# Optimization experiments

Hardware: AMD Instinct MI355X
Metric: run time of the kernel (lower is better)

Reference implementation:

```python
import jax, jax.numpy as jnp
import numpy as np

B, T, DMODEL = 8, 1024, 1024
N_HEADS, DK, DV = 16, 64, 64
FF_INNER = 4096


def setup_inputs() -> dict:
    key = jax.random.key(0)
    ks = jax.random.split(key, 9)
    s = 0.02  # init scale so softmax logits stay sane
    return {
        "x": jax.random.normal(ks[0], (B, T, DMODEL), dtype=jnp.float32),
        "Wq": jax.random.normal(ks[1], (N_HEADS, DMODEL, DK), dtype=jnp.float32) * s,
        "Wk": jax.random.normal(ks[2], (N_HEADS, DMODEL, DK), dtype=jnp.float32) * s,
        "Wv": jax.random.normal(ks[3], (N_HEADS, DMODEL, DV), dtype=jnp.float32) * s,
        "Wo": jax.random.normal(ks[4], (DMODEL, DMODEL), dtype=jnp.float32) * s,
        "W1": jax.random.normal(ks[5], (FF_INNER, DMODEL), dtype=jnp.float32) * s,
        "b1": jax.random.normal(ks[6], (FF_INNER,), dtype=jnp.float32) * s,
        "W2": jax.random.normal(ks[7], (DMODEL, FF_INNER), dtype=jnp.float32) * s,
        "b2": jax.random.normal(ks[8], (DMODEL,), dtype=jnp.float32) * s,
    }


def _pseudo_norm(y):
    # Original: y - mean - std (unbiased std, torch default). NOT a real layernorm.
    mean = jnp.mean(y, axis=-1, keepdims=True)
    std = jnp.std(y, axis=-1, keepdims=True, ddof=1)
    return y - mean - std


def reference(x, Wq, Wk, Wv, Wo, W1, b1, W2, b2):
    dk = Wq.shape[-1]
    # per-head projections: (B,T,D) x (H,D,dk) -> (B,H,T,dk)
    WQ = jnp.einsum("btd,hdk->bhtk", x, Wq)
    WK = jnp.einsum("btd,hdk->bhtk", x, Wk)
    WV = jnp.einsum("btd,hdv->bhtv", x, Wv)
    scores = jnp.einsum("bhqk,bhsk->bhqs", WQ, WK) / np.sqrt(dk).astype(np.float32)
    # Faithful to original: softmax over dim=2, i.e. the QUERY axis of (B,H,Tq,Tk)
    attn = jax.nn.softmax(scores, axis=2)
    part = jnp.einsum("bhqs,bhsv->bhqv", attn, WV)  # (B,H,T,dv)
    # concat heads: (B,T,H*dv) == (B,T,dmodel)
    part = part.transpose(0, 2, 1, 3).reshape(part.shape[0], part.shape[2], -1)
    out1 = part @ Wo + x
    out1 = _pseudo_norm(out1)
    # FeedForward: Linear(dmodel->inner), relu, Linear(inner->dmodel)
    h = jnp.maximum(out1 @ W1.T + b1, 0.0)
    out2 = h @ W2.T + b2 + out1
    return _pseudo_norm(out2)
```

## Files before the change

### kernel.cpp

```cpp
#include <hip/hip_runtime.h>
#include <math.h>


#define B_ 8
#define T_ 1024
#define D_ 1024
#define H_ 16
#define DK_ 64
#define FF_ 4096
#define M_ (B_ * T_)

typedef unsigned short u16;
typedef __attribute__((ext_vector_type(8))) short bf16x8;
typedef __attribute__((ext_vector_type(4))) float f32x4;

#define QSZ 8388608ull

__device__ __forceinline__ float b2f(u16 u) {
  union { unsigned int i; float f; } x;
  x.i = ((unsigned int)u) << 16;
  return x.f;
}
__device__ __forceinline__ u16 f2b(float f) {
  union { float f; unsigned int i; } x;
  x.f = f;
  unsigned int r = (x.i + 0x7FFFu + ((x.i >> 16) & 1u)) >> 16;
  return (u16)r;
}
__device__ __forceinline__ float fexp2(float x) {
#if __has_builtin(__builtin_amdgcn_exp2f)
  return __builtin_amdgcn_exp2f(x);
#else
  return exp2f(x);
#endif
}
#define C_QK 0.1803368801111244f

typedef __attribute__((address_space(1))) const void gas_void;
typedef __attribute__((address_space(3))) void las_void;
__device__ __forceinline__ void gload16(const void* g, void* l) {
  __builtin_amdgcn_global_load_lds((gas_void*)g, (las_void*)l, 16, 0, 0);
}

template <int EPI>
__global__ __launch_bounds__(256) void gemm16_k(
    const u16* __restrict__ A, const u16* __restrict__ Bt,
    int M, int N, int K, int lda, int ldb,
    float* __restrict__ C, int ldc, u16* __restrict__ Cb,
    const float* __restrict__ res, const float* __restrict__ bias) {
  __shared__ __align__(16) u16 As[2][128 * 32];
  __shared__ __align__(16) u16 Bs[2][128 * 32];

  const int tid = threadIdx.x;
  const int lane = tid & 63, wv = tid >> 6;
  const int m0 = blockIdx.y * 128, n0 = blockIdx.x * 128;
  const int wr = (wv >> 1) * 64, wc = (wv & 1) * 64;

  f32x4 acc[4][4];
#pragma unroll
  for (int i = 0; i < 4; ++i)
#pragma unroll
    for (int j = 0; j < 4; ++j) acc[i][j] = (f32x4){0.f, 0.f, 0.f, 0.f};

  const int srow = wv * 16 + (lane >> 2);
  const int scol = (lane & 3) * 8;
  const int fr = lane & 15, fk = (lane >> 4) * 8;

  const u16* gA0 = &A[(size_t)(m0 + srow) * lda + scol];
  const u16* gA1 = &A[(size_t)(m0 + srow + 64) * lda + scol];
  const u16* gB0 = &Bt[(size_t)(n0 + srow) * ldb + scol];
  const u16* gB1 = &Bt[(size_t)(n0 + srow + 64) * ldb + scol];

  gload16(gA0, &As[0][wv * 512]);
  gload16(gA1, &As[0][2048 + wv * 512]);
  gload16(gB0, &Bs[0][wv * 512]);
  gload16(gB1, &Bs[0][2048 + wv * 512]);
  __syncthreads();

  int cur = 0;
  for (int k0 = 0; k0 < K; k0 += 32) {
    if (k0 + 32 < K) {
      int nx = cur ^ 1, ko = k0 + 32;
      gload16(gA0 + ko, &As[nx][wv * 512]);
      gload16(gA1 + ko, &As[nx][2048 + wv * 512]);
      gload16(gB0 + ko, &Bs[nx][wv * 512]);
      gload16(gB1 + ko, &Bs[nx][2048 + wv * 512]);
    }
    bf16x8 af[4], bfr[4];
#pragma unroll
    for (int mi = 0; mi < 4; ++mi)
      af[mi] = *(const bf16x8*)&As[cur][(wr + mi * 16 + fr) * 32 + fk];
#pragma unroll
    for (int ni = 0; ni < 4; ++ni)
      bfr[ni] = *(const bf16x8*)&Bs[cur][(wc + ni * 16 + fr) * 32 + fk];
#pragma unroll
    for (int mi = 0; mi < 4; ++mi)
#pragma unroll
      for (int ni = 0; ni < 4; ++ni)
        acc[mi][ni] = __builtin_amdgcn_mfma_f32_16x16x32_bf16(
            af[mi], bfr[ni], acc[mi][ni], 0, 0, 0);
    __syncthreads();
    cur ^= 1;
  }

  const int fq = (lane >> 4) * 4;
#pragma unroll
  for (int mi = 0; mi < 4; ++mi) {
#pragma unroll
    for (int ni = 0; ni < 4; ++ni) {
      const int row = m0 + wr + mi * 16 + fq;
      const int col = n0 + wc + ni * 16 + fr;
      f32x4 v = acc[mi][ni];
      if (EPI == 6) {
        const int seg = col >> 10, cl = col & 1023;
        if (seg < 2) {
          u16* dst = Cb + (size_t)seg * QSZ;
#pragma unroll
          for (int r = 0; r < 4; ++r)
            dst[(size_t)(row + r) * 1024 + cl] = f2b(v[r]);
        } else {
          ushort4 w;
          w.x = f2b(v[0]); w.y = f2b(v[1]); w.z = f2b(v[2]); w.w = f2b(v[3]);
          size_t vidx = 2 * QSZ +
                        (((size_t)(row >> 10) * 16 + (cl >> 6)) * 64 +
                         (cl & 63)) * (size_t)T_ + (row & 1023);
          *(ushort4*)&Cb[vidx] = w;
        }
      } else {
#pragma unroll
        for (int r = 0; r < 4; ++r) {
          float val = v[r];
          size_t idx = (size_t)(row + r) * ldc + col;
          if (EPI == 1) {
            C[idx] = val + res[idx];
          } else if (EPI == 2) {
            Cb[idx] = f2b(fmaxf(val + bias[col], 0.f));
          } else if (EPI == 3) {
            C[idx] = val + bias[col] + res[idx];
          } else if (EPI == 4) {
            C[idx] = C[idx] + val;
          }
        }
      }
    }
  }
}

__global__ __launch_bounds__(256) void cvt_k(const float* __restrict__ in,
                                             u16* __restrict__ out, int n4) {
  int i = blockIdx.x * 256 + threadIdx.x;
  if (i >= n4) return;
  float4 v = *(const float4*)&in[(size_t)i * 4];
  ushort4 o;
  o.x = f2b(v.x); o.y = f2b(v.y); o.z = f2b(v.z); o.w = f2b(v.w);
  *(ushort4*)&out[(size_t)i * 4] = o;
}

__global__ __launch_bounds__(256) void tconv_k(const float* __restrict__ src,
                                               u16* __restrict__ dst, int R,
                                               int C) {
  __shared__ __align__(16) float t[32][33];
  const size_t bo = (size_t)blockIdx.z * R * C;
  const int r0 = blockIdx.y * 32, c0 = blockIdx.x * 32;
  const int tid = threadIdx.x;
  const int row = tid >> 3, c4 = (tid & 7) * 4;
  float4 v = *(const float4*)&src[bo + (size_t)(r0 + row) * C + c0 + c4];
  t[row][c4 + 0] = v.x; t[row][c4 + 1] = v.y;
  t[row][c4 + 2] = v.z; t[row][c4 + 3] = v.w;
  __syncthreads();
  ushort4 o;
  o.x = f2b(t[c4 + 0][row]); o.y = f2b(t[c4 + 1][row]);
  o.z = f2b(t[c4 + 2][row]); o.w = f2b(t[c4 + 3][row]);
  *(ushort4*)&dst[bo + (size_t)(c0 + row) * R + r0 + c4] = o;
}

__global__ __launch_bounds__(256) void attn_lsum_k(
    const u16* __restrict__ q, const u16* __restrict__ k,
    float* __restrict__ Lg) {
  __shared__ __align__(16) u16 Qs[128 * 64];
  __shared__ float Lsh[2][128];
  const int tid = threadIdx.x, lane = tid & 63, wv = tid >> 6;
  const int s0 = blockIdx.x * 128, h = blockIdx.y, b = blockIdx.z;
  const int bh = b * H_ + h;
  const u16* qbase = q + (size_t)b * T_ * D_ + h * DK_;
  const u16* kbase = k + (size_t)b * T_ * D_ + h * DK_;

  const int wr = (wv >> 1) * 64, wc = (wv & 1) * 64;
  const int fr = lane & 15, fs8 = (lane >> 4) * 8, fq = (lane >> 4) * 4;

  bf16x8 kf[4][2];
#pragma unroll
  for (int mi = 0; mi < 4; ++mi)
#pragma unroll
    for (int ks = 0; ks < 2; ++ks)
      kf[mi][ks] = *(const bf16x8*)&kbase[(size_t)(s0 + wr + mi * 16 + fr) * D_ +
                                          ks * 32 + fs8];

  float lrun[4][4];
#pragma unroll
  for (int mi = 0; mi < 4; ++mi)
#pragma unroll
    for (int r = 0; r < 4; ++r) lrun[mi][r] = 0.f;

  const int srow = wv * 8 + (lane >> 3);
  const int sscol = ((lane & 7) ^ ((lane >> 3) & 7)) * 8;

  for (int q0 = 0; q0 < T_; q0 += 128) {
    __syncthreads();
#pragma unroll
    for (int it = 0; it < 4; ++it)
      gload16(&qbase[(size_t)(q0 + it * 32 + srow) * D_ + sscol],
              &Qs[(it * 32 + wv * 8) * 64]);
    __syncthreads();

    f32x4 acc[4][4];
#pragma unroll
    for (int mi = 0; mi < 4; ++mi)
#pragma unroll
      for (int ni = 0; ni < 4; ++ni) acc[mi][ni] = (f32x4){0.f, 0.f, 0.f, 0.f};

#pragma unroll
    for (int ks = 0; ks < 2; ++ks) {
      bf16x8 qf[4];
#pragma unroll
      for (int ni = 0; ni < 4; ++ni) {
        int qr = wc + ni * 16 + fr;
        int slot = (ks * 4 + (lane >> 4)) ^ (qr & 7);
        qf[ni] = *(const bf16x8*)&Qs[qr * 64 + slot * 8];
      }
#pragma unroll
      for (int mi = 0; mi < 4; ++mi)
#pragma unroll
        for (int ni = 0; ni < 4; ++ni)
          acc[mi][ni] = __builtin_amdgcn_mfma_f32_16x16x32_bf16(
              kf[mi][ks], qf[ni], acc[mi][ni], 0, 0, 0);
    }
#pragma unroll
    for (int mi = 0; mi < 4; ++mi)
#pragma unroll
      for (int r = 0; r < 4; ++r) {
        float e = 0.f;
#pragma unroll
        for (int ni = 0; ni < 4; ++ni) e += fexp2(acc[mi][ni][r] * C_QK);
        lrun[mi][r] += e;
      }
  }

#pragma unroll
  for (int mi = 0; mi < 4; ++mi)
#pragma unroll
    for (int r = 0; r < 4; ++r) {
      float s = lrun[mi][r];
      s += __shfl_xor(s, 1, 64); s += __shfl_xor(s, 2, 64);
      s += __shfl_xor(s, 4, 64); s += __shfl_xor(s, 8, 64);
      if (fr == 0) Lsh[wv & 1][wr + mi * 16 + fq + r] = s;
    }
  __syncthreads();
  if (tid < 128)
    Lg[(size_t)bh * T_ + s0 + tid] = -__log2f(Lsh[0][tid] + Lsh[1][tid]);
}

__global__ __launch_bounds__(256) void attn_pv_k(
    const u16* __restrict__ q, const u16* __restrict__ k,
    const u16* __restrict__ vt, const float* __restrict__ Lg,
    u16* __restrict__ part) {
  __shared__ __align__(16) u16 Ks[128 * 64];
  __shared__ __align__(16) u16 Vs[64 * 128];
  __shared__ __align__(16) u16 Ps[128 * 128];
  const int tid = threadIdx.x, lane = tid & 63, wv = tid >> 6;
  const int q0 = blockIdx.x * 128, h = blockIdx.y, b = blockIdx.z;
  const int bh = b * H_ + h;
  const u16* qbase = q + (size_t)b * T_ * D_ + h * DK_;
  const u16* kbase = k + (size_t)b * T_ * D_ + h * DK_;
  const u16* vtb = vt + (size_t)bh * DK_ * T_;
  const float* lb = Lg + (size_t)bh * T_;

  const int wr = (wv >> 1) * 64, wc = (wv & 1) * 64;
  const int fr = lane & 15, fs8 = (lane >> 4) * 8, fq = (lane >> 4) * 4;

  bf16x8 qf[4][2];
#pragma unroll
  for (int mi = 0; mi < 4; ++mi)
#pragma unroll
    for (int ks = 0; ks < 2; ++ks)
      qf[mi][ks] = *(const bf16x8*)&qbase[(size_t)(q0 + wr + mi * 16 + fr) * D_ +
                                          ks * 32 + fs8];

  f32x4 acc2[2][4];
#pragma unroll
  for (int i = 0; i < 2; ++i)
#pragma unroll
    for (int j = 0; j < 4; ++j) acc2[i][j] = (f32x4){0.f, 0.f, 0.f, 0.f};

  const int ksrow = wv * 8 + (lane >> 3);
  const int kscol = ((lane & 7) ^ ((lane >> 3) & 7)) * 8;

  for (int s0 = 0; s0 < T_; s0 += 128) {
    __syncthreads();
#pragma unroll
    for (int it = 0; it < 4; ++it)
      gload16(&kbase[(size_t)(s0 + it * 32 + ksrow) * D_ + kscol],
              &Ks[(it * 32 + wv * 8) * 64]);
#pragma unroll
    for (int it = 0; it < 4; ++it) {
      int v = it * 16 + wv * 4 + (lane >> 4);
      int sslot = (lane & 15) ^ (v & 7);
      gload16(&vtb[(size_t)v * T_ + s0 + sslot * 8],
              &Vs[(it * 16 + wv * 4) * 128]);
    }
    __syncthreads();

    f32x4 accs[4][4];
#pragma unroll
    for (int mi = 0; mi < 4; ++mi)
#pragma unroll
      for (int ni = 0; ni < 4; ++ni) accs[mi][ni] = (f32x4){0.f, 0.f, 0.f, 0.f};
#pragma unroll
    for (int ks = 0; ks < 2; ++ks) {
      bf16x8 kfr[4];
#pragma unroll
      for (int ni = 0; ni < 4; ++ni) {
        int sr = wc + ni * 16 + fr;
        int slot = (ks * 4 + (lane >> 4)) ^ (sr & 7);
        kfr[ni] = *(const bf16x8*)&Ks[sr * 64 + slot * 8];
      }
#pragma unroll
      for (int mi = 0; mi < 4; ++mi)
#pragma unroll
        for (int ni = 0; ni < 4; ++ni)
          accs[mi][ni] = __builtin_amdgcn_mfma_f32_16x16x32_bf16(
              qf[mi][ks], kfr[ni], accs[mi][ni], 0, 0, 0);
    }

#pragma unroll
    for (int ni = 0; ni < 4; ++ni) {
      float lg = lb[s0 + wc + ni * 16 + fr];
      int scol = wc + ni * 16 + fr;
#pragma unroll
      for (int mi = 0; mi < 4; ++mi) {
#pragma unroll
        for (int r = 0; r < 4; ++r) {
          int qrow = wr + mi * 16 + fq + r;
          u16 pv = f2b(fexp2(fmaf(accs[mi][ni][r], C_QK, lg)));
          int eoff = qrow * 128 + ((((scol << 1) ^ ((qrow & 7) << 4))) >> 1);
          Ps[eoff] = pv;
        }
      }
    }
    __syncthreads();

#pragma unroll
    for (int ks2 = 0; ks2 < 4; ++ks2) {
      bf16x8 pa[2], vb2[4];
#pragma unroll
      for (int mi2 = 0; mi2 < 2; ++mi2) {
        int qr = wv * 32 + mi2 * 16 + fr;
        int slot = (ks2 * 4 + (lane >> 4)) ^ (qr & 7);
        pa[mi2] = *(const bf16x8*)&Ps[qr * 128 + slot * 8];
      }
#pragma unroll
      for (int ni2 = 0; ni2 < 4; ++ni2) {
        int v = ni2 * 16 + fr;
        int slot = (ks2 * 4 + (lane >> 4)) ^ (v & 7);
        vb2[ni2] = *(const bf16x8*)&Vs[v * 128 + slot * 8];
      }
#pragma unroll
      for (int mi2 = 0; mi2 < 2; ++mi2)
#pragma unroll
        for (int ni2 = 0; ni2 < 4; ++ni2)
          acc2[mi2][ni2] = __builtin_amdgcn_mfma_f32_16x16x32_bf16(
              pa[mi2], vb2[ni2], acc2[mi2][ni2], 0, 0, 0);
    }
  }

#pragma unroll
  for (int mi2 = 0; mi2 < 2; ++mi2)
#pragma unroll
    for (int ni2 = 0; ni2 < 4; ++ni2)
#pragma unroll
      for (int r = 0; r < 4; ++r) {
        int qrow = q0 + wv * 32 + mi2 * 16 + fq + r;
        int v = ni2 * 16 + fr;
        part[(size_t)(b * T_ + qrow) * D_ + h * DK_ + v] =
            f2b(acc2[mi2][ni2][r]);
      }
}

template <bool WB>
__global__ __launch_bounds__(256) void norm_k(const float* __restrict__ in,
                                              float* __restrict__ out,
                                              u16* __restrict__ ob) {
  __shared__ float red[8];
  const int row = blockIdx.x, tid = threadIdx.x;
  float4 vv = *(const float4*)&in[(size_t)row * D_ + tid * 4];
  float s = vv.x + vv.y + vv.z + vv.w;
  for (int off = 1; off < 64; off <<= 1) s += __shfl_xor(s, off, 64);
  if ((tid & 63) == 0) red[tid >> 6] = s;
  __syncthreads();
  float mean = (red[0] + red[1] + red[2] + red[3]) * (1.f / 1024.f);
  float dx = vv.x - mean, dy = vv.y - mean, dz = vv.z - mean, dw = vv.w - mean;
  float s2 = dx * dx + dy * dy + dz * dz + dw * dw;
  __syncthreads();
  for (int off = 1; off < 64; off <<= 1) s2 += __shfl_xor(s2, off, 64);
  if ((tid & 63) == 0) red[4 + (tid >> 6)] = s2;
  __syncthreads();
  float var = (red[4] + red[5] + red[6] + red[7]) * (1.f / 1023.f);
  float sd = sqrtf(var);
  float4 o = {dx - sd, dy - sd, dz - sd, dw - sd};
  *(float4*)&out[(size_t)row * D_ + tid * 4] = o;
  if (WB) {
    ushort4 q;
    q.x = f2b(o.x); q.y = f2b(o.y); q.z = f2b(o.z); q.w = f2b(o.w);
    *(ushort4*)&ob[(size_t)row * D_ + tid * 4] = q;
  }
}

extern "C" void kernel_launch(void* const* d_in, const int* in_sizes, int n_in,
                              void* d_out, int out_size, void* d_ws,
                              size_t ws_size, hipStream_t stream) {
  const float* x  = (const float*)d_in[0];
  const float* Wq = (const float*)d_in[1];
  const float* Wk = (const float*)d_in[2];
  const float* Wv = (const float*)d_in[3];
  const float* Wo = (const float*)d_in[4];
  const float* W1 = (const float*)d_in[5];
  const float* b1 = (const float*)d_in[6];
  const float* W2 = (const float*)d_in[7];
  const float* b2 = (const float*)d_in[8];

  char* w = (char*)d_ws;
  u16* qb16   = (u16*)(w + (0ull << 20));
  u16* kb16   = (u16*)(w + (16ull << 20));
  u16* Vt     = (u16*)(w + (32ull << 20));
  u16* xb     = (u16*)(w + (48ull << 20));
  u16* part16 = (u16*)(w + (64ull << 20));
  u16* Wqkv   = (u16*)(w + (80ull << 20));
  u16* Wot    = (u16*)(w + (86ull << 20));
  u16* W1b    = (u16*)(w + (88ull << 20));
  u16* W2b    = (u16*)(w + (96ull << 20));
  float* Lg   = (float*)(w + (104ull << 20));
  u16* o1b = qb16;
  u16* hc  = kb16;
  float* o1 = (float*)d_out;

  dim3 thr(256);

  int n4x = (M_ * D_) / 4;
  cvt_k<<<dim3((n4x + 255) / 256), thr, 0, stream>>>(x, xb, n4x);
  tconv_k<<<dim3(2, 32, 16), thr, 0, stream>>>(Wq, Wqkv, 1024, 64);
  tconv_k<<<dim3(2, 32, 16), thr, 0, stream>>>(Wk, Wqkv + 1048576, 1024, 64);
  tconv_k<<<dim3(2, 32, 16), thr, 0, stream>>>(Wv, Wqkv + 2097152, 1024, 64);
  tconv_k<<<dim3(32, 32, 1), thr, 0, stream>>>(Wo, Wot, 1024, 1024);
  int n4w = (FF_ * D_) / 4;
  cvt_k<<<dim3((n4w + 255) / 256), thr, 0, stream>>>(W1, W1b, n4w);
  cvt_k<<<dim3((n4w + 255) / 256), thr, 0, stream>>>(W2, W2b, n4w);

  gemm16_k<6><<<dim3(3072 / 128, M_ / 128), thr, 0, stream>>>(
      xb, Wqkv, M_, 3072, D_, D_, D_, nullptr, D_, qb16, nullptr, nullptr);

  dim3 ga(T_ / 128, H_, B_);
  attn_lsum_k<<<ga, thr, 0, stream>>>(qb16, kb16, Lg);
  attn_pv_k<<<ga, thr, 0, stream>>>(qb16, kb16, Vt, Lg, part16);

  gemm16_k<1><<<dim3(D_ / 128, M_ / 128), thr, 0, stream>>>(
      part16, Wot, M_, D_, D_, D_, D_, o1, D_, nullptr, x, nullptr);
  norm_k<true><<<dim3(M_), thr, 0, stream>>>(o1, o1, o1b);

  for (int c = 0; c < 2; ++c) {
    const u16* W1c = W1b + (size_t)c * 2048 * 1024;
    const u16* W2c = W2b + (size_t)c * 2048;
    gemm16_k<2><<<dim3(2048 / 128, M_ / 128), thr, 0, stream>>>(
        o1b, W1c, M_, 2048, 1024, 1024, 1024, nullptr, 2048, hc, nullptr,
        b1 + c * 2048);
    if (c == 0) {
      gemm16_k<3><<<dim3(D_ / 128, M_ / 128), thr, 0, stream>>>(
          hc, W2c, M_, 1024, 2048, 2048, FF_, o1, D_, nullptr, o1, b2);
    } else {
      gemm16_k<4><<<dim3(D_ / 128, M_ / 128), thr, 0, stream>>>(
          hc, W2c, M_, 1024, 2048, 2048, FF_, o1, D_, nullptr, nullptr, nullptr);
    }
  }

  norm_k<false><<<dim3(M_), thr, 0, stream>>>(o1, o1, nullptr);
}
```

Measured before the change: 649.2 us.

## Fold softmax column normalizer into V and transpose score MFMA for packed P stores

Instead of adding -log2(L) inside every exponent in the PV kernel, the lsum kernel now stores the reciprocal column sums and a new pass pre-scales V^T by them in place. The score MFMA operands are swapped so each lane holds four consecutive key positions, letting P be written to LDS as packed 8-byte stores with a new XOR swizzle instead of scalar 2-byte stores. It also swaps the manual bf16 rounding for the HIP intrinsic. The extra elementwise pass over V and the extra bf16 rounding of scaled V add traffic and slight numerical change.

```diff
diff --git a/kernel.cpp b/kernel.cpp
--- a/kernel.cpp
+++ b/kernel.cpp
@@ -1,4 +1,5 @@
 #include <hip/hip_runtime.h>
+#include <hip/hip_bf16.h>
 #include <math.h>
 
 
@@ -22,10 +23,8 @@
   return x.f;
 }
 __device__ __forceinline__ u16 f2b(float f) {
-  union { float f; unsigned int i; } x;
-  x.f = f;
-  unsigned int r = (x.i + 0x7FFFu + ((x.i >> 16) & 1u)) >> 16;
-  return (u16)r;
+  __hip_bfloat16 h = __float2bfloat16(f);
+  return *(u16*)&h;
 }
 __device__ __forceinline__ float fexp2(float x) {
 #if __has_builtin(__builtin_amdgcn_exp2f)
@@ -176,7 +175,7 @@
 
 __global__ __launch_bounds__(256) void attn_lsum_k(
     const u16* __restrict__ q, const u16* __restrict__ k,
-    float* __restrict__ Lg) {
+    float* __restrict__ Lrcp) {
   __shared__ __align__(16) u16 Qs[128 * 64];
   __shared__ float Lsh[2][128];
   const int tid = threadIdx.x, lane = tid & 63, wv = tid >> 6;
@@ -257,13 +256,31 @@
     }
   __syncthreads();
   if (tid < 128)
-    Lg[(size_t)bh * T_ + s0 + tid] = -__log2f(Lsh[0][tid] + Lsh[1][tid]);
+    Lrcp[(size_t)bh * T_ + s0 + tid] = 1.f / (Lsh[0][tid] + Lsh[1][tid]);
+}
+
+__global__ __launch_bounds__(256) void vscale_k(u16* __restrict__ vt,
+                                                const float* __restrict__ Lrcp) {
+  int i8 = blockIdx.x * 256 + threadIdx.x;
+  size_t base = (size_t)i8 * 8;
+  int bh = (int)(base >> 16);
+  int s = (int)(base & 1023);
+  float4 r0 = *(const float4*)&Lrcp[(size_t)bh * 1024 + s];
+  float4 r1 = *(const float4*)&Lrcp[(size_t)bh * 1024 + s + 4];
+  ushort4 a = *(const ushort4*)&vt[base];
+  ushort4 c = *(const ushort4*)&vt[base + 4];
+  ushort4 oa, oc;
+  oa.x = f2b(b2f(a.x) * r0.x); oa.y = f2b(b2f(a.y) * r0.y);
+  oa.z = f2b(b2f(a.z) * r0.z); oa.w = f2b(b2f(a.w) * r0.w);
+  oc.x = f2b(b2f(c.x) * r1.x); oc.y = f2b(b2f(c.y) * r1.y);
+  oc.z = f2b(b2f(c.z) * r1.z); oc.w = f2b(b2f(c.w) * r1.w);
+  *(ushort4*)&vt[base] = oa;
+  *(ushort4*)&vt[base + 4] = oc;
 }
 
 __global__ __launch_bounds__(256) void attn_pv_k(
     const u16* __restrict__ q, const u16* __restrict__ k,
-    const u16* __restrict__ vt, const float* __restrict__ Lg,
-    u16* __restrict__ part) {
+    const u16* __restrict__ vt, u16* __restrict__ part) {
   __shared__ __align__(16) u16 Ks[128 * 64];
   __shared__ __align__(16) u16 Vs[64 * 128];
   __shared__ __align__(16) u16 Ps[128 * 128];
@@ -273,17 +290,16 @@
   const u16* qbase = q + (size_t)b * T_ * D_ + h * DK_;
   const u16* kbase = k + (size_t)b * T_ * D_ + h * DK_;
   const u16* vtb = vt + (size_t)bh * DK_ * T_;
-  const float* lb = Lg + (size_t)bh * T_;
 
   const int wr = (wv >> 1) * 64, wc = (wv & 1) * 64;
   const int fr = lane & 15, fs8 = (lane >> 4) * 8, fq = (lane >> 4) * 4;
 
   bf16x8 qf[4][2];
 #pragma unroll
-  for (int mi = 0; mi < 4; ++mi)
+  for (int ni = 0; ni < 4; ++ni)
 #pragma unroll
     for (int ks = 0; ks < 2; ++ks)
-      qf[mi][ks] = *(const bf16x8*)&qbase[(size_t)(q0 + wr + mi * 16 + fr) * D_ +
+      qf[ni][ks] = *(const bf16x8*)&qbase[(size_t)(q0 + wc + ni * 16 + fr) * D_ +
                                           ks * 32 + fs8];
 
   f32x4 acc2[2][4];
@@ -310,41 +326,43 @@
     }
     __syncthreads();
 
-    f32x4 accs[4][4];
+    f32x4 st[4][4];
 #pragma unroll
     for (int mi = 0; mi < 4; ++mi)
 #pragma unroll
-      for (int ni = 0; ni < 4; ++ni) accs[mi][ni] = (f32x4){0.f, 0.f, 0.f, 0.f};
+      for (int ni = 0; ni < 4; ++ni) st[mi][ni] = (f32x4){0.f, 0.f, 0.f, 0.f};
 #pragma unroll
     for (int ks = 0; ks < 2; ++ks) {
-      bf16x8 kfr[4];
-#pragma unroll
-      for (int ni = 0; ni < 4; ++ni) {
-        int sr = wc + ni * 16 + fr;
+      bf16x8 kfa[4];
+#pragma unroll
+      for (int mi = 0; mi < 4; ++mi) {
+        int sr = wr + mi * 16 + fr;
         int slot = (ks * 4 + (lane >> 4)) ^ (sr & 7);
-        kfr[ni] = *(const bf16x8*)&Ks[sr * 64 + slot * 8];
+        kfa[mi] = *(const bf16x8*)&Ks[sr * 64 + slot * 8];
       }
 #pragma unroll
       for (int mi = 0; mi < 4; ++mi)
 #pragma unroll
         for (int ni = 0; ni < 4; ++ni)
-          accs[mi][ni] = __builtin_amdgcn_mfma_f32_16x16x32_bf16(
-              qf[mi][ks], kfr[ni], accs[mi][ni], 0, 0, 0);
+          st[mi][ni] = __builtin_amdgcn_mfma_f32_16x16x32_bf16(
+              kfa[mi], qf[ni][ks], st[mi][ni], 0, 0, 0);
     }
 
 #pragma unroll
     for (int ni = 0; ni < 4; ++ni) {
-      float lg = lb[s0 + wc + ni * 16 + fr];
-      int scol = wc + ni * 16 + fr;
+      int qcol = wc + ni * 16 + fr;
 #pragma unroll
       for (int mi = 0; mi < 4; ++mi) {
-#pragma unroll
-        for (int r = 0; r < 4; ++r) {
-          int qrow = wr + mi * 16 + fq + r;
-          u16 pv = f2b(fexp2(fmaf(accs[mi][ni][r], C_QK, lg)));
-          int eoff = qrow * 128 + ((((scol << 1) ^ ((qrow & 7) << 4))) >> 1);
-          Ps[eoff] = pv;
-        }
+        int sb = wr + mi * 16 + fq;
+        u16 e0 = f2b(fexp2(st[mi][ni][0] * C_QK));
+        u16 e1 = f2b(fexp2(st[mi][ni][1] * C_QK));
+        u16 e2 = f2b(fexp2(st[mi][ni][2] * C_QK));
+        u16 e3 = f2b(fexp2(st[mi][ni][3] * C_QK));
+        uint2 w;
+        w.x = (unsigned int)e0 | ((unsigned int)e1 << 16);
+        w.y = (unsigned int)e2 | ((unsigned int)e3 << 16);
+        int byte = qcol * 256 + ((sb * 2) ^ ((qcol & 15) << 4));
+        *(uint2*)((char*)Ps + byte) = w;
       }
     }
     __syncthreads();
@@ -355,8 +373,8 @@
 #pragma unroll
       for (int mi2 = 0; mi2 < 2; ++mi2) {
         int qr = wv * 32 + mi2 * 16 + fr;
-        int slot = (ks2 * 4 + (lane >> 4)) ^ (qr & 7);
-        pa[mi2] = *(const bf16x8*)&Ps[qr * 128 + slot * 8];
+        int byte = qr * 256 + (((ks2 * 32 + (lane >> 4) * 8) * 2) ^ ((qr & 15) << 4));
+        pa[mi2] = *(const bf16x8*)((const char*)Ps + byte);
       }
 #pragma unroll
       for (int ni2 = 0; ni2 < 4; ++ni2) {
@@ -438,7 +456,7 @@
   u16* Wot    = (u16*)(w + (86ull << 20));
   u16* W1b    = (u16*)(w + (88ull << 20));
   u16* W2b    = (u16*)(w + (96ull << 20));
-  float* Lg   = (float*)(w + (104ull << 20));
+  float* Lrcp = (float*)(w + (104ull << 20));
   u16* o1b = qb16;
   u16* hc  = kb16;
   float* o1 = (float*)d_out;
@@ -459,8 +477,9 @@
       xb, Wqkv, M_, 3072, D_, D_, D_, nullptr, D_, qb16, nullptr, nullptr);
 
   dim3 ga(T_ / 128, H_, B_);
-  attn_lsum_k<<<ga, thr, 0, stream>>>(qb16, kb16, Lg);
-  attn_pv_k<<<ga, thr, 0, stream>>>(qb16, kb16, Vt, Lg, part16);
+  attn_lsum_k<<<ga, thr, 0, stream>>>(qb16, kb16, Lrcp);
+  vscale_k<<<dim3((int)(QSZ / 8 / 256)), thr, 0, stream>>>(Vt, Lrcp);
+  attn_pv_k<<<ga, thr, 0, stream>>>(qb16, kb16, Vt, part16);
 
   gemm16_k<1><<<dim3(D_ / 128, M_ / 128), thr, 0, stream>>>(
       part16, Wot, M_, D_, D_, D_, D_, o1, D_, nullptr, x, nullptr);
```

Measured after the change: 613.3 us. 1.06x faster.
